# Kernel tuning notes

Measured on AMD Instinct MI355X. Metric: run time of the kernel, lower is better.

Reference implementation:

```python
import jax, jax.numpy as jnp
import numpy as np
from jax import lax

B, H, L, DK = 8, 8, 1024, 64
BN_EPS = 1e-5


def _conv_bn_sm(x, w, b, g, beta, pad):
    # x: [B, H, L] (N=batch, C=h heads as channels, spatial=L)
    y = lax.conv_general_dilated(x, w, (1,), [(pad, pad)], dimension_numbers=("NCH", "OIH", "NCH"))
    y = y + b[None, :, None]
    # BatchNorm1d in training mode: batch stats over (N, L) per channel, biased var
    mu = jnp.mean(y, axis=(0, 2), keepdims=True)
    var = jnp.var(y, axis=(0, 2), keepdims=True)
    y = (y - mu) * (g[None, :, None] / jnp.sqrt(var + BN_EPS)) + beta[None, :, None]
    return jax.nn.softmax(y, axis=-1)


def setup_inputs() -> dict:
    key = jax.random.key(0)
    ks = jax.random.split(key, 20)
    n = lambda i, shape, s=1.0: jax.random.normal(ks[i], shape, dtype=jnp.float32) * s
    inp = {
        "Q": n(0, (B, H, L, DK)),
        "K": n(1, (B, H, L, DK)),
        "V": n(2, (B, H, L, DK)),
        "attn_mask": jnp.ones((1,), dtype=bool),
        # proj_q / proj_k: Linear(d_k, 1, bias=False) weight [1, d_k] -> stored as [d_k]
        "wq": n(3, (DK,), 0.1), "wk": n(4, (DK,), 0.1),
        # proj_back_q / proj_back_k: Linear(1, d_k, bias=False) weight [d_k, 1] -> [d_k]
        "wbq": n(5, (DK,), 0.1), "wbk": n(6, (DK,), 0.1),
        # Conv1d(h, h, f) weights [out=h, in=h, f] + bias [h]
        "cq3_w": n(7, (H, H, 3), 0.2), "cq3_b": n(8, (H,), 0.05),
        "cq9_w": n(9, (H, H, 9), 0.1), "cq9_b": n(10, (H,), 0.05),
        "ck3_w": n(11, (H, H, 3), 0.2), "ck3_b": n(12, (H,), 0.05),
        "ck9_w": n(13, (H, H, 9), 0.1), "ck9_b": n(14, (H,), 0.05),
        # BatchNorm1d affine params
        "bnq3_g": jnp.ones((H,), jnp.float32), "bnq3_b": jnp.zeros((H,), jnp.float32),
        "bnq9_g": jnp.ones((H,), jnp.float32), "bnq9_b": jnp.zeros((H,), jnp.float32),
        "bnk3_g": jnp.ones((H,), jnp.float32), "bnk3_b": jnp.zeros((H,), jnp.float32),
        "bnk9_g": jnp.ones((H,), jnp.float32), "bnk9_b": jnp.zeros((H,), jnp.float32),
    }
    return inp


def reference(Q, K, V, attn_mask, wq, wk, wbq, wbk,
              cq3_w, cq3_b, cq9_w, cq9_b, ck3_w, ck3_b, ck9_w, ck9_b,
              bnq3_g, bnq3_b, bnq9_g, bnq9_b, bnk3_g, bnk3_b, bnk9_g, bnk9_b):
    b, h, l, d_k = Q.shape
    l_k = K.shape[2]
    # proj to scalar per position, reshape to [b, h, l]
    Qp = jnp.einsum("bhld,d->bhl", Q, wq)
    Kp = jnp.einsum("bhld,d->bhl", K, wk)
    # multi-scale conv + BN(train) + softmax branches
    q0 = _conv_bn_sm(Qp, cq3_w, cq3_b, bnq3_g, bnq3_b, 1)
    q1 = _conv_bn_sm(Qp, cq9_w, cq9_b, bnq9_g, bnq9_b, 4)
    k0 = _conv_bn_sm(Kp, ck3_w, ck3_b, bnk3_g, bnk3_b, 1)
    k1 = _conv_bn_sm(Kp, ck9_w, ck9_b, bnk9_g, bnk9_b, 4)
    # faithful to torch: cat along dim 0 then C-order reshape to [b,h,l,2], max over last
    Qm = jnp.max(jnp.concatenate([q0, q1], axis=0).reshape(b, h, l, 2), axis=-1)
    Km = jnp.max(jnp.concatenate([k0, k1], axis=0).reshape(b, h, l_k, 2), axis=-1)
    # proj back 1 -> d_k (no bias): outer with weight vector
    Qn = Qm[..., None] * wbq  # [b,h,l,d_k]
    Kn = Km[..., None] * wbk  # [b,h,l_k,d_k]
    scores = jnp.einsum("bhqd,bhkd->bhqk", Qn, Kn) / jnp.sqrt(jnp.float32(d_k))
    attn = jax.nn.softmax(scores, axis=-1)
    context = jnp.einsum("bhqk,bhkd->bhqd", attn, V)
    return (context, attn)
```

## Files before the change

### kernel.cpp

```cpp
#include <hip/hip_runtime.h>

constexpr int SL = 1024;
constexpr int NBH = 64;

constexpr int QP_OFF = 0;
constexpr int KP_OFF = 65536;
constexpr int Y_OFF  = 131072;
constexpr int QM_OFF = 655360;
constexpr int KM_OFF = 720896;
constexpr int ST_OFF = 786432;
constexpr int C_OFF  = 786496;
constexpr int VT_OFF = 786560;

typedef __attribute__((ext_vector_type(8))) short short8;
typedef __attribute__((ext_vector_type(4))) float f32x4;

__device__ inline unsigned short f2bf(float x) {
    unsigned int u = __float_as_uint(x);
    unsigned int r = (u + 0x7fff + ((u >> 16) & 1)) >> 16;
    return (unsigned short)r;
}

__global__ __launch_bounds__(256) void k_projpack(
    const float* __restrict__ Q, const float* __restrict__ K,
    const float* __restrict__ V,
    const float* __restrict__ wq, const float* __restrict__ wk,
    const float* __restrict__ wbq, const float* __restrict__ wbk,
    float* __restrict__ ws)
{
    int b = blockIdx.x;
    int tid = threadIdx.x;
    if (b < 8192) {
        bool isQ = b < 4096;
        const float* src = isQ ? Q : K;
        const float* w   = isQ ? wq : wk;
        int row = (b - (isQ ? 0 : 4096)) * 16 + (tid >> 4);
        int l16 = tid & 15;
        float4 x  = ((const float4*)(src + row * 64))[l16];
        float4 w4 = ((const float4*)w)[l16];
        float v = x.x * w4.x + x.y * w4.y + x.z * w4.z + x.w * w4.w;
        #pragma unroll
        for (int m = 8; m; m >>= 1) v += __shfl_xor(v, m);
        if (l16 == 0) ws[(isQ ? QP_OFF : KP_OFF) + row] = v;
    } else if (b < 10240) {
        int t = (b - 8192) * 256 + tid;
        int lane = t & 63;
        int s    = (t >> 6) & 7;
        int dsub = (t >> 9) & 3;
        int chunk= (t >> 11) & 3;
        int bh   = t >> 13;
        const float* vb = V + bh * (SL * 64);
        int k0 = chunk * 256 + s * 32 + (lane >> 4) * 8;
        int d  = dsub * 16 + (lane & 15);
        unsigned short o[8];
        #pragma unroll
        for (int j = 0; j < 8; j++) o[j] = f2bf(vb[(k0 + j) * 64 + d]);
        unsigned short* vt = (unsigned short*)(ws + VT_OFF);
        *(short8*)(vt + (size_t)t * 8) = *(short8*)o;
    } else {
        if (tid < 64) {
            float v = wbq[tid] * wbk[tid];
            #pragma unroll
            for (int m = 32; m; m >>= 1) v += __shfl_xor(v, m);
            if (tid == 0) ws[C_OFF] = v * 0.125f;
        }
    }
}

__global__ __launch_bounds__(256) void k_conv(
    float* __restrict__ ws,
    const float* __restrict__ w0, const float* __restrict__ b0,
    const float* __restrict__ w1, const float* __restrict__ b1,
    const float* __restrict__ w2, const float* __restrict__ b2,
    const float* __restrict__ w3, const float* __restrict__ b3)
{
    int branch = blockIdx.x >> 6;
    int n = (blockIdx.x >> 3) & 7;
    int seg = blockIdx.x & 7;
    int t0 = seg * 128;
    const float* wp = branch == 0 ? w0 : branch == 1 ? w1 : branch == 2 ? w2 : w3;
    const float* bp = branch == 0 ? b0 : branch == 1 ? b1 : branch == 2 ? b2 : b3;
    const int F = (branch & 1) ? 9 : 3;
    const int PAD = F >> 1;
    const float* x = ws + ((branch < 2) ? QP_OFF : KP_OFF) + n * 8 * SL;

    __shared__ float xl[8][136];
    __shared__ float wl[8 * 8 * 9];
    __shared__ float bl[8];
    int tid = threadIdx.x;
    for (int i = tid; i < 8 * 8 * F; i += 256) wl[i] = wp[i];
    if (tid < 8) bl[tid] = bp[tid];
    for (int i = tid; i < 8 * 136; i += 256) {
        int ci = i / 136; int tt = i - ci * 136;
        int ta = t0 + tt - 4;
        xl[ci][tt] = (ta >= 0 && ta < SL) ? x[ci * SL + ta] : 0.f;
    }
    __syncthreads();
    int c = tid >> 5, u = tid & 31;
    float s1 = 0.f, s2 = 0.f;
    float* yout = ws + Y_OFF + branch * (NBH * SL) + (n * 8 + c) * SL + t0;
    float res[4];
    #pragma unroll
    for (int q = 0; q < 4; q++) {
        int tl = u * 4 + q;
        float acc = bl[c];
        for (int ci = 0; ci < 8; ci++) {
            const float* xr = &xl[ci][tl + 4 - PAD];
            const float* wr = &wl[(c * 8 + ci) * F];
            for (int f = 0; f < F; f++) acc += wr[f] * xr[f];
        }
        res[q] = acc;
        s1 += acc; s2 += acc * acc;
    }
    *(float4*)&yout[u * 4] = make_float4(res[0], res[1], res[2], res[3]);
    #pragma unroll
    for (int m = 16; m; m >>= 1) {
        s1 += __shfl_xor(s1, m);
        s2 += __shfl_xor(s2, m);
    }
    if (u == 0) {
        atomicAdd(&ws[ST_OFF + (branch * 8 + c) * 2],     s1);
        atomicAdd(&ws[ST_OFF + (branch * 8 + c) * 2 + 1], s2);
    }
}

__global__ __launch_bounds__(256) void k_bnmix(
    float* __restrict__ ws,
    const float* __restrict__ g0, const float* __restrict__ be0,
    const float* __restrict__ g1, const float* __restrict__ be1,
    const float* __restrict__ g2, const float* __restrict__ be2,
    const float* __restrict__ g3, const float* __restrict__ be3)
{
    int blk = blockIdx.x;
    int which = blk >> 6;
    int i = (blk >> 3) & 7, j = blk & 7;
    int n = 2 * i + (j >= 4 ? 1 : 0);
    int br = which * 2 + (n >= 8 ? 1 : 0);
    int row = n & 7;
    int tid = threadIdx.x;
    int half = tid >> 7;
    int u = tid & 127;
    int c = 2 * (j & 3) + half;
    const float* gp = br == 0 ? g0 : br == 1 ? g1 : br == 2 ? g2 : g3;
    const float* bp = br == 0 ? be0 : br == 1 ? be1 : br == 2 ? be2 : be3;
    float s1 = ws[ST_OFF + (br * 8 + c) * 2];
    float s2 = ws[ST_OFF + (br * 8 + c) * 2 + 1];
    float mu  = s1 * (1.f / 8192.f);
    float var = s2 * (1.f / 8192.f) - mu * mu;
    float sc = gp[c] * rsqrtf(var + 1e-5f);
    float sh = bp[c] - mu * sc;
    const float* y = ws + Y_OFF + br * (NBH * SL) + (row * 8 + c) * SL;
    float4 ya = ((const float4*)y)[u * 2];
    float4 yb = ((const float4*)y)[u * 2 + 1];
    float z[8] = { ya.x * sc + sh, ya.y * sc + sh, ya.z * sc + sh, ya.w * sc + sh,
                   yb.x * sc + sh, yb.y * sc + sh, yb.z * sc + sh, yb.w * sc + sh };
    float mx = z[0];
    #pragma unroll
    for (int q = 1; q < 8; q++) mx = fmaxf(mx, z[q]);
    __shared__ float r1[4], r2[4];
    #pragma unroll
    for (int m = 32; m; m >>= 1) mx = fmaxf(mx, __shfl_xor(mx, m));
    if ((tid & 63) == 0) r1[tid >> 6] = mx;
    __syncthreads();
    mx = half ? fmaxf(r1[2], r1[3]) : fmaxf(r1[0], r1[1]);
    float e[8];
    float s = 0.f;
    #pragma unroll
    for (int q = 0; q < 8; q++) { e[q] = __expf(z[q] - mx); s += e[q]; }
    #pragma unroll
    for (int m = 32; m; m >>= 1) s += __shfl_xor(s, m);
    if ((tid & 63) == 0) r2[tid >> 6] = s;
    __syncthreads();
    s = half ? (r2[2] + r2[3]) : (r2[0] + r2[1]);
    float inv = 1.f / s;
    float4 o = make_float4(fmaxf(e[0], e[1]) * inv, fmaxf(e[2], e[3]) * inv,
                           fmaxf(e[4], e[5]) * inv, fmaxf(e[6], e[7]) * inv);
    float* outp = ws + (which ? KM_OFF : QM_OFF) + i * 8192 + j * 1024 + half * 512;
    ((float4*)outp)[u] = o;
}

__global__ __launch_bounds__(256) void k_attn(
    float* __restrict__ out, const float* __restrict__ ws)
{
    int bh = blockIdx.x >> 4;
    int qt = blockIdx.x & 15;
    int tid = threadIdx.x;
    __shared__ float kml[1024];
    __shared__ float aq[64], mq[64], rq[64];
    __shared__ unsigned short bpk[4 * 8 * 64 * 8];
    __shared__ float red[256];
    __shared__ float rmx[4], rmn[4];

    const float* km = ws + KM_OFF + bh * SL;
    const float* qm = ws + QM_OFF + bh * SL + qt * 64;
    float c = ws[C_OFF];

    float lmax = -1e30f, lmin = 1e30f;
    #pragma unroll
    for (int i = 0; i < 4; i++) {
        float v = km[tid + 256 * i];
        kml[tid + 256 * i] = v;
        lmax = fmaxf(lmax, v); lmin = fminf(lmin, v);
    }
    #pragma unroll
    for (int m = 32; m; m >>= 1) {
        lmax = fmaxf(lmax, __shfl_xor(lmax, m));
        lmin = fminf(lmin, __shfl_xor(lmin, m));
    }
    if ((tid & 63) == 0) { rmx[tid >> 6] = lmax; rmn[tid >> 6] = lmin; }
    __syncthreads();
    float kmax = fmaxf(fmaxf(rmx[0], rmx[1]), fmaxf(rmx[2], rmx[3]));
    float kmin = fminf(fminf(rmn[0], rmn[1]), fminf(rmn[2], rmn[3]));
    if (tid < 64) {
        float a = c * qm[tid];
        aq[tid] = a;
        mq[tid] = (a > 0.f) ? a * kmax : a * kmin;
    }
    __syncthreads();
    {
        int q = tid >> 2, g = tid & 3;
        float a = aq[q], m = mq[q];
        float s = 0.f;
        const float* kp = kml + g * 256;
        for (int k = 0; k < 256; k++) s += __expf(a * kp[k] - m);
        red[tid] = s;
        __syncthreads();
        if (tid < 64) {
            float d = red[tid * 4] + red[tid * 4 + 1] + red[tid * 4 + 2] + red[tid * 4 + 3];
            rq[tid] = 1.f / d;
        }
        __syncthreads();
    }

    int w = tid >> 6, lane = tid & 63;
    int m16 = lane & 15, kg = lane >> 4;
    int qloc = w * 16 + m16;
    float a = aq[qloc], mm = mq[qloc], rr = rq[qloc];
    float* attn_row = out + 4194304 + ((size_t)(bh * SL + qt * 64 + qloc)) * SL;
    const uint4* vt4 = (const uint4*)((const unsigned short*)(ws + VT_OFF) + (size_t)bh * 4 * 16384);

    f32x4 acc0 = {0,0,0,0}, acc1 = {0,0,0,0}, acc2 = {0,0,0,0}, acc3 = {0,0,0,0};

    for (int ch = 0; ch < 4; ch++) {
        const uint4* src = vt4 + ch * 2048;
        uint4* dst = (uint4*)bpk;
        #pragma unroll
        for (int i = 0; i < 8; i++) dst[tid + 256 * i] = src[tid + 256 * i];
        __syncthreads();

        #pragma unroll
        for (int s = 0; s < 8; s++) {
            int k0 = ch * 256 + s * 32 + kg * 8;
            const float* kp = kml + k0;
            float e[8];
            #pragma unroll
            for (int j = 0; j < 8; j++) e[j] = __expf(a * kp[j] - mm) * rr;
            *(float4*)(attn_row + k0)     = make_float4(e[0], e[1], e[2], e[3]);
            *(float4*)(attn_row + k0 + 4) = make_float4(e[4], e[5], e[6], e[7]);
            unsigned short af[8];
            #pragma unroll
            for (int j = 0; j < 8; j++) af[j] = f2bf(e[j]);
            short8 av = *(short8*)af;
            const short8* bbase = (const short8*)bpk + s * 64 + lane;
            short8 b0 = bbase[0 * 512];
            short8 b1 = bbase[1 * 512];
            short8 b2 = bbase[2 * 512];
            short8 b3 = bbase[3 * 512];
            acc0 = __builtin_amdgcn_mfma_f32_16x16x32_bf16(av, b0, acc0, 0, 0, 0);
            acc1 = __builtin_amdgcn_mfma_f32_16x16x32_bf16(av, b1, acc1, 0, 0, 0);
            acc2 = __builtin_amdgcn_mfma_f32_16x16x32_bf16(av, b2, acc2, 0, 0, 0);
            acc3 = __builtin_amdgcn_mfma_f32_16x16x32_bf16(av, b3, acc3, 0, 0, 0);
        }
        __syncthreads();
    }
    float* ctx = out + ((size_t)(bh * SL + qt * 64 + w * 16)) * 64;
    #pragma unroll
    for (int reg = 0; reg < 4; reg++) {
        int row = kg * 4 + reg;
        float* cp = ctx + row * 64 + m16;
        cp[0]  = acc0[reg];
        cp[16] = acc1[reg];
        cp[32] = acc2[reg];
        cp[48] = acc3[reg];
    }
}

extern "C" void kernel_launch(void* const* d_in, const int* in_sizes, int n_in,
                              void* d_out, int out_size, void* d_ws, size_t ws_size,
                              hipStream_t stream)
{
    const float* Q      = (const float*)d_in[0];
    const float* K      = (const float*)d_in[1];
    const float* V      = (const float*)d_in[2];
    const float* wq     = (const float*)d_in[4];
    const float* wk     = (const float*)d_in[5];
    const float* wbq    = (const float*)d_in[6];
    const float* wbk    = (const float*)d_in[7];
    const float* cq3_w  = (const float*)d_in[8];
    const float* cq3_b  = (const float*)d_in[9];
    const float* cq9_w  = (const float*)d_in[10];
    const float* cq9_b  = (const float*)d_in[11];
    const float* ck3_w  = (const float*)d_in[12];
    const float* ck3_b  = (const float*)d_in[13];
    const float* ck9_w  = (const float*)d_in[14];
    const float* ck9_b  = (const float*)d_in[15];
    const float* bnq3_g = (const float*)d_in[16];
    const float* bnq3_b = (const float*)d_in[17];
    const float* bnq9_g = (const float*)d_in[18];
    const float* bnq9_b = (const float*)d_in[19];
    const float* bnk3_g = (const float*)d_in[20];
    const float* bnk3_b = (const float*)d_in[21];
    const float* bnk9_g = (const float*)d_in[22];
    const float* bnk9_b = (const float*)d_in[23];
    float* out = (float*)d_out;
    float* ws  = (float*)d_ws;

    (void)hipMemsetAsync(ws + ST_OFF, 0, 64 * sizeof(float), stream);

    k_projpack<<<10241, 256, 0, stream>>>(Q, K, V, wq, wk, wbq, wbk, ws);
    k_conv<<<256, 256, 0, stream>>>(ws, cq3_w, cq3_b, cq9_w, cq9_b,
                                    ck3_w, ck3_b, ck9_w, ck9_b);
    k_bnmix<<<128, 256, 0, stream>>>(ws, bnq3_g, bnq3_b, bnq9_g, bnq9_b,
                                     bnk3_g, bnk3_b, bnk9_g, bnk9_b);
    k_attn<<<1024, 256, 0, stream>>>(out, ws);
}
```

Baseline: 410.0 us.

## Read V fragments directly from global, swizzle blocks per XCD, drop memset

The attention kernel no longer stages the bf16 V tiles through shared memory with block barriers. Each wave now loads its MFMA B fragments straight from global memory, and blocks are remapped so that the 16 query tiles of one head land on the same XCD to share L2. The memset of the BN statistics is folded into the projection kernel, and the conv output store becomes coalesced scalar stores. The key loads in the exp loops are vectorised to float4. The cost is repeated global/L2 reads of V per wave instead of one shared-memory copy per block.

Result: no change. 412.7 us (+0.7%).

```diff
diff --git a/kernel.cpp b/kernel.cpp
--- a/kernel.cpp
+++ b/kernel.cpp
@@ -59,6 +59,7 @@
         *(short8*)(vt + (size_t)t * 8) = *(short8*)o;
     } else {
         if (tid < 64) {
+            ws[ST_OFF + tid] = 0.f;
             float v = wbq[tid] * wbk[tid];
             #pragma unroll
             for (int m = 32; m; m >>= 1) v += __shfl_xor(v, m);
@@ -99,20 +100,18 @@
     int c = tid >> 5, u = tid & 31;
     float s1 = 0.f, s2 = 0.f;
     float* yout = ws + Y_OFF + branch * (NBH * SL) + (n * 8 + c) * SL + t0;
-    float res[4];
     #pragma unroll
     for (int q = 0; q < 4; q++) {
-        int tl = u * 4 + q;
+        int tl = q * 32 + u;
         float acc = bl[c];
         for (int ci = 0; ci < 8; ci++) {
             const float* xr = &xl[ci][tl + 4 - PAD];
             const float* wr = &wl[(c * 8 + ci) * F];
             for (int f = 0; f < F; f++) acc += wr[f] * xr[f];
         }
-        res[q] = acc;
+        yout[tl] = acc;
         s1 += acc; s2 += acc * acc;
     }
-    *(float4*)&yout[u * 4] = make_float4(res[0], res[1], res[2], res[3]);
     #pragma unroll
     for (int m = 16; m; m >>= 1) {
         s1 += __shfl_xor(s1, m);
@@ -182,12 +181,13 @@
 __global__ __launch_bounds__(256) void k_attn(
     float* __restrict__ out, const float* __restrict__ ws)
 {
-    int bh = blockIdx.x >> 4;
-    int qt = blockIdx.x & 15;
+    int p = blockIdx.x;
+    int xcd = p & 7, jj = p >> 3;
+    int bh = xcd + 8 * (jj >> 4);
+    int qt = jj & 15;
     int tid = threadIdx.x;
     __shared__ float kml[1024];
     __shared__ float aq[64], mq[64], rq[64];
-    __shared__ unsigned short bpk[4 * 8 * 64 * 8];
     __shared__ float red[256];
     __shared__ float rmx[4], rmn[4];
 
@@ -221,8 +221,12 @@
         int q = tid >> 2, g = tid & 3;
         float a = aq[q], m = mq[q];
         float s = 0.f;
-        const float* kp = kml + g * 256;
-        for (int k = 0; k < 256; k++) s += __expf(a * kp[k] - m);
+        const float4* kp4 = ((const float4*)kml) + g * 64;
+        for (int k = 0; k < 64; k++) {
+            float4 kv = kp4[k];
+            s += __expf(a * kv.x - m) + __expf(a * kv.y - m)
+               + __expf(a * kv.z - m) + __expf(a * kv.w - m);
+        }
         red[tid] = s;
         __syncthreads();
         if (tid < 64) {
@@ -237,31 +241,34 @@
     int qloc = w * 16 + m16;
     float a = aq[qloc], mm = mq[qloc], rr = rq[qloc];
     float* attn_row = out + 4194304 + ((size_t)(bh * SL + qt * 64 + qloc)) * SL;
-    const uint4* vt4 = (const uint4*)((const unsigned short*)(ws + VT_OFF) + (size_t)bh * 4 * 16384);
+    const short8* vt8 = (const short8*)((const unsigned short*)(ws + VT_OFF))
+                        + (size_t)bh * 8192;
 
     f32x4 acc0 = {0,0,0,0}, acc1 = {0,0,0,0}, acc2 = {0,0,0,0}, acc3 = {0,0,0,0};
 
     for (int ch = 0; ch < 4; ch++) {
-        const uint4* src = vt4 + ch * 2048;
-        uint4* dst = (uint4*)bpk;
-        #pragma unroll
-        for (int i = 0; i < 8; i++) dst[tid + 256 * i] = src[tid + 256 * i];
-        __syncthreads();
-
+        const short8* vch = vt8 + ch * 2048;
         #pragma unroll
         for (int s = 0; s < 8; s++) {
             int k0 = ch * 256 + s * 32 + kg * 8;
-            const float* kp = kml + k0;
+            const float4* kp = (const float4*)(kml + k0);
+            float4 ka = kp[0], kb = kp[1];
             float e[8];
-            #pragma unroll
-            for (int j = 0; j < 8; j++) e[j] = __expf(a * kp[j] - mm) * rr;
+            e[0] = __expf(a * ka.x - mm) * rr;
+            e[1] = __expf(a * ka.y - mm) * rr;
+            e[2] = __expf(a * ka.z - mm) * rr;
+            e[3] = __expf(a * ka.w - mm) * rr;
+            e[4] = __expf(a * kb.x - mm) * rr;
+            e[5] = __expf(a * kb.y - mm) * rr;
+            e[6] = __expf(a * kb.z - mm) * rr;
+            e[7] = __expf(a * kb.w - mm) * rr;
             *(float4*)(attn_row + k0)     = make_float4(e[0], e[1], e[2], e[3]);
             *(float4*)(attn_row + k0 + 4) = make_float4(e[4], e[5], e[6], e[7]);
             unsigned short af[8];
             #pragma unroll
             for (int j = 0; j < 8; j++) af[j] = f2bf(e[j]);
             short8 av = *(short8*)af;
-            const short8* bbase = (const short8*)bpk + s * 64 + lane;
+            const short8* bbase = vch + s * 64 + lane;
             short8 b0 = bbase[0 * 512];
             short8 b1 = bbase[1 * 512];
             short8 b2 = bbase[2 * 512];
@@ -271,7 +278,6 @@
             acc2 = __builtin_amdgcn_mfma_f32_16x16x32_bf16(av, b2, acc2, 0, 0, 0);
             acc3 = __builtin_amdgcn_mfma_f32_16x16x32_bf16(av, b3, acc3, 0, 0, 0);
         }
-        __syncthreads();
     }
     float* ctx = out + ((size_t)(bh * SL + qt * 64 + w * 16)) * 64;
     #pragma unroll
@@ -315,8 +321,6 @@
     float* out = (float*)d_out;
     float* ws  = (float*)d_ws;
 
-    (void)hipMemsetAsync(ws + ST_OFF, 0, 64 * sizeof(float), stream);
-
     k_projpack<<<10241, 256, 0, stream>>>(Q, K, V, wq, wk, wbq, wbk, ws);
     k_conv<<<256, 256, 0, stream>>>(ws, cq3_w, cq3_b, cq9_w, cq9_b,
                                     ck3_w, ck3_b, ck9_w, ck9_b);
```
